# Kernel optimization log

Measured on AMD Instinct MI355X. Metric: run time of the kernel, lower is better.

## Reference

```python
import jax, jax.numpy as jnp
import numpy as np

N_NODES = 50000
GAMMA = -0.5
ZETA = 1.1
DEBUG_VAR = 1e-07


def setup_inputs() -> dict:
    key = jax.random.key(0)
    ks = jax.random.split(key, 8)
    N, E, D, H = N_NODES, 800000, 256, 128
    s = 0.05
    return {
        "x": jax.random.normal(ks[0], (N, D), jnp.float32),
        "W_nb": jax.random.normal(ks[1], (D, H), jnp.float32) * s,
        "b_nb": jnp.zeros((H,), jnp.float32),
        "W_self": jax.random.normal(ks[2], (D, H), jnp.float32) * s,
        "b_self": jnp.zeros((H,), jnp.float32),
        "W_att": jax.random.normal(ks[3], (2 * H, 1), jnp.float32) * s,
        "b_att": jnp.zeros((1,), jnp.float32),
        "values": jax.random.uniform(ks[4], (E,), jnp.float32),
        "noise": jax.random.uniform(ks[5], (E, 1), jnp.float32),
        "row": jax.random.randint(ks[6], (E,), 0, N, jnp.int32),
        "col": jax.random.randint(ks[7], (E,), 0, N, jnp.int32),
    }


def reference(x, W_nb, b_nb, W_self, b_self, W_att, b_att, values, noise, row, col):
    # edge gather + tiny attention MLP
    f1 = jax.nn.relu(x[row] @ W_nb + b_nb)      # [E, H]
    f2 = jax.nn.relu(x[col] @ W_self + b_self)  # [E, H]
    log_alpha = jnp.concatenate([f1, f2], axis=1) @ W_att + b_att  # [E, 1]

    # hard-concrete sample (training=True), beta=1.0
    u = noise + DEBUG_VAR
    gate = jax.nn.sigmoid(jnp.log(u) - jnp.log(1.0 - u) + log_alpha)
    mask = jnp.clip(gate * (ZETA - GAMMA) + GAMMA, 0.0, 1.0)[:, 0]  # [E]

    masked_values = values * mask

    # degree-normalized scatter: rowsum then symmetric D^{-1/2} A D^{-1/2}
    rowsum = jax.ops.segment_sum(masked_values, row, num_segments=N_NODES) + 1e-10
    d_inv_sqrt = jnp.power(rowsum, -0.5)
    d_inv_sqrt = jnp.where(jnp.isinf(d_inv_sqrt), 0.0, d_inv_sqrt)

    norm_values = masked_values * d_inv_sqrt[row] * d_inv_sqrt[col]  # [E]
    return norm_values
```

## Files before the change

kernel.cpp:

```cpp
#include <hip/hip_runtime.h>
#include <hip/hip_bf16.h>

typedef __attribute__((ext_vector_type(8))) short bf16x8;
typedef __attribute__((ext_vector_type(4))) float f32x4;

#define D_DIM 256
#define H_DIM 128
#define QSH 12544
#define NSL 64
#define NMAXL (4 * QSH)

__device__ inline ushort f2bf(float f) {
    union { float f; unsigned u; } a; a.f = f;
    unsigned r = a.u + 0x7fffu + ((a.u >> 16) & 1u);
    return (ushort)(r >> 16);
}
__device__ inline float bf2f(unsigned hi16) {
    union { unsigned u; float f; } a; a.u = hi16 << 16;
    return a.f;
}

__global__ void k0_init(const float* __restrict__ W_nb, const float* __restrict__ W_self,
                        ushort* __restrict__ Wt, float* __restrict__ dis, int N, int init_dis) {
    int i = blockIdx.x * 256 + threadIdx.x;
    if (i < 2 * H_DIM * D_DIM) {
        int j    = i & 7;
        int lane = (i >> 3) & 63;
        int ks   = (i >> 9) & 7;
        int ni   = (i >> 12) & 3;
        int cg   = i >> 14;
        int li   = lane & 15;
        int grp  = lane >> 4;
        int h    = (cg & 1) * 64 + ni * 16 + li;
        int k    = ks * 32 + grp * 8 + j;
        const float* W = (cg >> 1) ? W_self : W_nb;
        Wt[i] = f2bf(W[k * H_DIM + h]);
    }
    if (init_dis && i < N) dis[i] = 1e-10f;
}

__global__ __launch_bounds__(512, 2) void k1_gemm(
    const float* __restrict__ x, const ushort* __restrict__ Wt,
    const float* __restrict__ b_nb, const float* __restrict__ b_self,
    const float* __restrict__ W_att,
    float* __restrict__ g_nb, float* __restrict__ g_self, int N, int ntiles)
{
    __shared__ __align__(16) ushort A_lds[64][264];
    __shared__ float part[2][2][64];

    const int t    = threadIdx.x;
    const int lane = t & 63;
    const int w    = t >> 6;
    const int rh   = w >> 2;
    const int cg   = w & 3;
    const int br   = cg >> 1;
    const int ch   = cg & 1;
    const int li   = lane & 15;
    const int grp  = lane >> 4;

    float bias[4], aw[4];
    #pragma unroll
    for (int ni = 0; ni < 4; ni++) {
        int hh = ch * 64 + ni * 16 + li;
        bias[ni] = br ? b_self[hh] : b_nb[hh];
        aw[ni]   = W_att[br * H_DIM + hh];
    }

    bf16x8 Bf[4][8];
    #pragma unroll
    for (int ni = 0; ni < 4; ni++)
        #pragma unroll
        for (int ks = 0; ks < 8; ks++)
            Bf[ni][ks] = *reinterpret_cast<const bf16x8*>(
                Wt + (((size_t)(cg * 4 + ni) * 8 + ks) << 9) + lane * 8);

    const int sr = t >> 3;
    const int sc = t & 7;

    for (int rt = blockIdx.x; rt < ntiles; rt += gridDim.x) {
        const int row0 = rt * 64;

        __syncthreads();
        {
            const int gr = row0 + sr;
            const bool v = gr < N;
            const float4* src = reinterpret_cast<const float4*>(x + (size_t)gr * D_DIM);
            #pragma unroll
            for (int j = 0; j < 8; j++) {
                int c4 = sc + j * 8;
                ushort4 o;
                if (v) {
                    float4 f = src[c4];
                    o.x = f2bf(f.x); o.y = f2bf(f.y); o.z = f2bf(f.z); o.w = f2bf(f.w);
                } else { o.x = 0; o.y = 0; o.z = 0; o.w = 0; }
                *reinterpret_cast<ushort4*>(&A_lds[sr][c4 * 4]) = o;
            }
        }
        __syncthreads();

        f32x4 acc[2][4];
        #pragma unroll
        for (int mi = 0; mi < 2; mi++)
            #pragma unroll
            for (int ni = 0; ni < 4; ni++) acc[mi][ni] = f32x4{0.f, 0.f, 0.f, 0.f};

        #pragma unroll
        for (int ks = 0; ks < 8; ks++) {
            bf16x8 af0 = *reinterpret_cast<const bf16x8*>(&A_lds[rh * 32 + li][ks * 32 + grp * 8]);
            bf16x8 af1 = *reinterpret_cast<const bf16x8*>(&A_lds[rh * 32 + 16 + li][ks * 32 + grp * 8]);
            #pragma unroll
            for (int ni = 0; ni < 4; ni++) {
                acc[0][ni] = __builtin_amdgcn_mfma_f32_16x16x32_bf16(af0, Bf[ni][ks], acc[0][ni], 0, 0, 0);
                acc[1][ni] = __builtin_amdgcn_mfma_f32_16x16x32_bf16(af1, Bf[ni][ks], acc[1][ni], 0, 0, 0);
            }
        }

        float p[2][4];
        #pragma unroll
        for (int mi = 0; mi < 2; mi++)
            #pragma unroll
            for (int r4 = 0; r4 < 4; r4++) p[mi][r4] = 0.f;
        #pragma unroll
        for (int ni = 0; ni < 4; ni++)
            #pragma unroll
            for (int mi = 0; mi < 2; mi++)
                #pragma unroll
                for (int r4 = 0; r4 < 4; r4++) {
                    float y = acc[mi][ni][r4] + bias[ni];
                    y = y > 0.f ? y : 0.f;
                    p[mi][r4] += y * aw[ni];
                }
        #pragma unroll
        for (int mi = 0; mi < 2; mi++)
            #pragma unroll
            for (int r4 = 0; r4 < 4; r4++) {
                float v = p[mi][r4];
                #pragma unroll
                for (int m = 1; m < 16; m <<= 1) v += __shfl_xor(v, m);
                if (li == 0)
                    part[br][ch][rh * 32 + mi * 16 + grp * 4 + r4] = v;
            }
        __syncthreads();

        if (t < 128) {
            int b_ = t >> 6, lr = t & 63;
            int gr = row0 + lr;
            if (gr < N) {
                float val = part[b_][0][lr] + part[b_][1][lr];
                if (b_) g_self[gr] = val; else g_nb[gr] = val;
            }
        }
    }
}

__global__ __launch_bounds__(256) void k2a_gate(
    const int* __restrict__ row, const int* __restrict__ col,
    const float* __restrict__ values, const float* __restrict__ noise,
    const float* __restrict__ g_nb, const float* __restrict__ g_self,
    const float* __restrict__ b_att, unsigned* __restrict__ pk, int E)
{
    int i = (blockIdx.x * 256 + threadIdx.x) * 2;
    if (i >= E) return;
    const float ba = b_att[0];
    if (i + 1 < E) {
        int2   r2 = *reinterpret_cast<const int2*>(row + i);
        int2   c2 = *reinterpret_cast<const int2*>(col + i);
        float2 v2 = *reinterpret_cast<const float2*>(values + i);
        float2 u2 = *reinterpret_cast<const float2*>(noise + i);
        float gn0 = g_nb[r2.x], gs0 = g_self[c2.x];
        float gn1 = g_nb[r2.y], gs1 = g_self[c2.y];
        float u0 = u2.x + 1e-7f, u1 = u2.y + 1e-7f;
        float la0 = gn0 + gs0 + ba, la1 = gn1 + gs1 + ba;
        float g0 = u0 / (u0 + (1.f - u0) * __expf(-la0));
        float g1 = u1 / (u1 + (1.f - u1) * __expf(-la1));
        float m0 = v2.x * fminf(fmaxf(g0 * 1.6f - 0.5f, 0.f), 1.f);
        float m1 = v2.y * fminf(fmaxf(g1 * 1.6f - 0.5f, 0.f), 1.f);
        uint2 o;
        o.x = ((unsigned)r2.x << 16) | (unsigned)f2bf(m0);
        o.y = ((unsigned)r2.y << 16) | (unsigned)f2bf(m1);
        *reinterpret_cast<uint2*>(pk + i) = o;
    } else {
        int e = i;
        int   r = row[e];
        float u    = noise[e] + 1e-7f;
        float la   = g_nb[r] + g_self[col[e]] + ba;
        float gate = u / (u + (1.f - u) * __expf(-la));
        float mask = fminf(fmaxf(gate * 1.6f - 0.5f, 0.f), 1.f);
        pk[e] = ((unsigned)r << 16) | (unsigned)f2bf(values[e] * mask);
    }
}

__global__ __launch_bounds__(1024) void k2q_scatter(
    const unsigned* __restrict__ pk, ushort* __restrict__ priv, int E, int ES)
{
    __shared__ float acc[QSH];
    const int s  = blockIdx.x >> 2;
    const int q  = blockIdx.x & 3;
    const int t  = threadIdx.x;
    const int lo = q * QSH;

    for (int i = t; i < QSH; i += 1024) acc[i] = 0.f;
    __syncthreads();

    const int base = s * ES;
    int end = base + ES; if (end > E) end = E;

    int i = base + t * 4;
    for (; i + 3 < end; i += 4096) {
        uint4 p4 = *reinterpret_cast<const uint4*>(pk + i);
        unsigned p; int d; float m;
        p = p4.x; d = (int)(p >> 16) - lo; m = bf2f(p & 0xffffu);
        if ((unsigned)d < (unsigned)QSH && m != 0.f) atomicAdd(&acc[d], m);
        p = p4.y; d = (int)(p >> 16) - lo; m = bf2f(p & 0xffffu);
        if ((unsigned)d < (unsigned)QSH && m != 0.f) atomicAdd(&acc[d], m);
        p = p4.z; d = (int)(p >> 16) - lo; m = bf2f(p & 0xffffu);
        if ((unsigned)d < (unsigned)QSH && m != 0.f) atomicAdd(&acc[d], m);
        p = p4.w; d = (int)(p >> 16) - lo; m = bf2f(p & 0xffffu);
        if ((unsigned)d < (unsigned)QSH && m != 0.f) atomicAdd(&acc[d], m);
    }
    for (; i < end; i++) {
        unsigned p = pk[i];
        int d = (int)(p >> 16) - lo;
        float m = bf2f(p & 0xffffu);
        if ((unsigned)d < (unsigned)QSH && m != 0.f) atomicAdd(&acc[d], m);
    }
    __syncthreads();

    ushort* dst = priv + (size_t)s * (4 * QSH) + lo;
    for (int j = t * 2; j < QSH; j += 2048) {
        unsigned pkk = (unsigned)f2bf(acc[j]) | ((unsigned)f2bf(acc[j + 1]) << 16);
        *reinterpret_cast<unsigned*>(dst + j) = pkk;
    }
}

__global__ __launch_bounds__(256) void k2c_reduce(
    const ushort* __restrict__ priv, ushort* __restrict__ disb, int N)
{
    int n0 = (blockIdx.x * 256 + threadIdx.x) * 2;
    if (n0 >= N) return;
    float s0 = 1e-10f, s1 = 1e-10f;
    for (int p = 0; p < NSL; p++) {
        unsigned v = *reinterpret_cast<const unsigned*>(priv + (size_t)p * (4 * QSH) + n0);
        s0 += bf2f(v & 0xffffu);
        s1 += bf2f(v >> 16);
    }
    unsigned o = (unsigned)f2bf(rsqrtf(s0)) | ((unsigned)f2bf(rsqrtf(s1)) << 16);
    *reinterpret_cast<unsigned*>(disb + n0) = o;
}

__global__ __launch_bounds__(1024) void k3_edge2_lds(
    const unsigned* __restrict__ pk, const int* __restrict__ col,
    float* __restrict__ out, const ushort* __restrict__ disb,
    int Npad2, int E, int EB)
{
    __shared__ ushort ldis[NMAXL];
    const int t = threadIdx.x;
    {
        const unsigned* src = reinterpret_cast<const unsigned*>(disb);
        unsigned* dst = reinterpret_cast<unsigned*>(ldis);
        const int nw = Npad2 >> 1;
        for (int i = t; i < nw; i += 1024) dst[i] = src[i];
    }
    __syncthreads();

    const int base = blockIdx.x * EB;
    int end = base + EB; if (end > E) end = E;

    int i = base + t * 4;
    for (; i + 3 < end; i += 4096) {
        uint4 p4 = *reinterpret_cast<const uint4*>(pk + i);
        int4  c4 = *reinterpret_cast<const int4*>(col + i);
        float4 o;
        o.x = bf2f(p4.x & 0xffffu) * bf2f(ldis[p4.x >> 16]) * bf2f(ldis[c4.x]);
        o.y = bf2f(p4.y & 0xffffu) * bf2f(ldis[p4.y >> 16]) * bf2f(ldis[c4.y]);
        o.z = bf2f(p4.z & 0xffffu) * bf2f(ldis[p4.z >> 16]) * bf2f(ldis[c4.z]);
        o.w = bf2f(p4.w & 0xffffu) * bf2f(ldis[p4.w >> 16]) * bf2f(ldis[c4.w]);
        *reinterpret_cast<float4*>(out + i) = o;
    }
    for (; i < end; i++) {
        unsigned p = pk[i];
        out[i] = bf2f(p & 0xffffu) * bf2f(ldis[p >> 16]) * bf2f(ldis[col[i]]);
    }
}

__global__ __launch_bounds__(256) void k2_atomic_fb(
    const int* __restrict__ row, const int* __restrict__ col,
    const float* __restrict__ values, const float* __restrict__ noise,
    const float* __restrict__ g_nb, const float* __restrict__ g_self,
    const float* __restrict__ b_att,
    float* __restrict__ out, float* __restrict__ dis, int E)
{
    int e = blockIdx.x * 256 + threadIdx.x;
    if (e >= E) return;
    int   r = row[e], c = col[e];
    float u = noise[e] + 1e-7f;
    float la = g_nb[r] + g_self[c] + b_att[0];
    float gate = u / (u + (1.f - u) * __expf(-la));
    float mask = fminf(fmaxf(gate * 1.6f - 0.5f, 0.f), 1.f);
    float m = values[e] * mask;
    out[e] = m;
    if (m != 0.f) atomicAdd(&dis[r], m);
}
__global__ __launch_bounds__(256) void k2c_rsqrt_fb(float* __restrict__ dis, int N)
{
    int n = blockIdx.x * 256 + threadIdx.x;
    if (n < N) dis[n] = rsqrtf(dis[n]);
}
__global__ __launch_bounds__(256) void k3_edge2_fb(
    const int* __restrict__ row, const int* __restrict__ col,
    float* __restrict__ out, const float* __restrict__ dis, int E)
{
    int e = blockIdx.x * 256 + threadIdx.x;
    if (e >= E) return;
    out[e] = out[e] * dis[row[e]] * dis[col[e]];
}

extern "C" void kernel_launch(void* const* d_in, const int* in_sizes, int n_in,
                              void* d_out, int out_size, void* d_ws, size_t ws_size,
                              hipStream_t stream) {
    const float* x      = (const float*)d_in[0];
    const float* W_nb   = (const float*)d_in[1];
    const float* b_nb   = (const float*)d_in[2];
    const float* W_self = (const float*)d_in[3];
    const float* b_self = (const float*)d_in[4];
    const float* W_att  = (const float*)d_in[5];
    const float* b_att  = (const float*)d_in[6];
    const float* values = (const float*)d_in[7];
    const float* noise  = (const float*)d_in[8];
    const int*   row    = (const int*)d_in[9];
    const int*   col    = (const int*)d_in[10];

    const int N = in_sizes[0] / D_DIM;
    const int E = in_sizes[7];
    float* out = (float*)d_out;

    char* ws = (char*)d_ws;
    ushort* Wt     = (ushort*)ws;
    float*  g_nb   = (float*)(ws + 131072);
    float*  g_self = g_nb + N;
    float*  dis    = g_self + N;
    ushort* disb   = (ushort*)dis;
    ushort* priv   = (ushort*)(dis + N);
    size_t pk_off  = 131072 + (size_t)3 * N * 4 + (size_t)NSL * NMAXL * 2;
    pk_off = (pk_off + 15) & ~(size_t)15;
    unsigned* pk   = (unsigned*)(ws + pk_off);

    const int Npad2 = (N + 1) & ~1;
    int ES = ((E + NSL - 1) / NSL + 3) & ~3;
    size_t need = pk_off + (size_t)E * 4;
    bool lds_path = (N <= NMAXL) && (need <= ws_size);

    int init_n = 2 * H_DIM * D_DIM;
    if (N > init_n) init_n = N;
    k0_init<<<(init_n + 255) / 256, 256, 0, stream>>>(W_nb, W_self, Wt, dis, N, lds_path ? 0 : 1);

    const int ntiles = (N + 63) / 64;
    k1_gemm<<<ntiles, 512, 0, stream>>>(x, Wt, b_nb, b_self, W_att, g_nb, g_self, N, ntiles);

    if (lds_path) {
        int eb2 = ((E + 1) / 2 + 255) / 256;
        k2a_gate<<<eb2, 256, 0, stream>>>(row, col, values, noise, g_nb, g_self,
                                          b_att, pk, E);
        k2q_scatter<<<NSL * 4, 1024, 0, stream>>>(pk, priv, E, ES);
        k2c_reduce<<<((N + 1) / 2 + 255) / 256, 256, 0, stream>>>(priv, disb, N);
        int EB = ((E + 255) / 256 + 3) & ~3;
        k3_edge2_lds<<<256, 1024, 0, stream>>>(pk, col, out, disb, Npad2, E, EB);
    } else {
        k2_atomic_fb<<<(E + 255) / 256, 256, 0, stream>>>(row, col, values, noise,
                                                          g_nb, g_self, b_att, out, dis, E);
        k2c_rsqrt_fb<<<(N + 255) / 256, 256, 0, stream>>>(dis, N);
        k3_edge2_fb<<<(E + 255) / 256, 256, 0, stream>>>(row, col, out, dis, E);
    }
}
```

Measured before the change: 64.58 us.

## Make GEMM kernel persistent with register-prefetched next tile of x

The node GEMM kernel now launches a fixed grid of 256 blocks that loop over row tiles, rather than one block per tile. While computing the current tile, each thread loads the next tile's x rows into registers, then converts them to bf16 and writes them to LDS after the epilogue, so global loads overlap MFMA work. The per-block cost of loading the weight fragments is also amortized over several tiles. The trade-off is extra register pressure from the 8 float4 staging registers, and fewer blocks available to hide memory latency.

```diff
diff --git a/kernel.cpp b/kernel.cpp
--- a/kernel.cpp
+++ b/kernel.cpp
@@ -57,6 +57,7 @@
     const int ch   = cg & 1;
     const int li   = lane & 15;
     const int grp  = lane >> 4;
+    const int G    = gridDim.x;
 
     float bias[4], aw[4];
     #pragma unroll
@@ -77,26 +78,41 @@
     const int sr = t >> 3;
     const int sc = t & 7;
 
-    for (int rt = blockIdx.x; rt < ntiles; rt += gridDim.x) {
+    int rt = blockIdx.x;
+    if (rt >= ntiles) return;
+
+    {
+        const int gr = rt * 64 + sr;
+        const bool v = gr < N;
+        const float4* src = reinterpret_cast<const float4*>(x + (size_t)gr * D_DIM);
+        #pragma unroll
+        for (int j = 0; j < 8; j++) {
+            ushort4 o;
+            if (v) {
+                float4 f = src[sc + j * 8];
+                o.x = f2bf(f.x); o.y = f2bf(f.y); o.z = f2bf(f.z); o.w = f2bf(f.w);
+            } else { o.x = 0; o.y = 0; o.z = 0; o.w = 0; }
+            *reinterpret_cast<ushort4*>(&A_lds[sr][(sc + j * 8) * 4]) = o;
+        }
+    }
+    __syncthreads();
+
+    for (; rt < ntiles; rt += G) {
         const int row0 = rt * 64;
-
-        __syncthreads();
-        {
-            const int gr = row0 + sr;
-            const bool v = gr < N;
+        const int nxt  = rt + G;
+        const bool have_next = nxt < ntiles;
+
+        float4 stn[8];
+        bool nv = false;
+        if (have_next) {
+            const int gr = nxt * 64 + sr;
+            nv = gr < N;
             const float4* src = reinterpret_cast<const float4*>(x + (size_t)gr * D_DIM);
-            #pragma unroll
-            for (int j = 0; j < 8; j++) {
-                int c4 = sc + j * 8;
-                ushort4 o;
-                if (v) {
-                    float4 f = src[c4];
-                    o.x = f2bf(f.x); o.y = f2bf(f.y); o.z = f2bf(f.z); o.w = f2bf(f.w);
-                } else { o.x = 0; o.y = 0; o.z = 0; o.w = 0; }
-                *reinterpret_cast<ushort4*>(&A_lds[sr][c4 * 4]) = o;
+            if (nv) {
+                #pragma unroll
+                for (int j = 0; j < 8; j++) stn[j] = src[sc + j * 8];
             }
         }
-        __syncthreads();
 
         f32x4 acc[2][4];
         #pragma unroll
@@ -150,6 +166,18 @@
                 if (b_) g_self[gr] = val; else g_nb[gr] = val;
             }
         }
+        if (have_next) {
+            #pragma unroll
+            for (int j = 0; j < 8; j++) {
+                ushort4 o;
+                if (nv) {
+                    float4 f = stn[j];
+                    o.x = f2bf(f.x); o.y = f2bf(f.y); o.z = f2bf(f.z); o.w = f2bf(f.w);
+                } else { o.x = 0; o.y = 0; o.z = 0; o.w = 0; }
+                *reinterpret_cast<ushort4*>(&A_lds[sr][(sc + j * 8) * 4]) = o;
+            }
+        }
+        __syncthreads();
     }
 }
 
@@ -355,7 +383,7 @@
     k0_init<<<(init_n + 255) / 256, 256, 0, stream>>>(W_nb, W_self, Wt, dis, N, lds_path ? 0 : 1);
 
     const int ntiles = (N + 63) / 64;
-    k1_gemm<<<ntiles, 512, 0, stream>>>(x, Wt, b_nb, b_self, W_att, g_nb, g_self, N, ntiles);
+    k1_gemm<<<256, 512, 0, stream>>>(x, Wt, b_nb, b_self, W_att, g_nb, g_self, N, ntiles);
 
     if (lds_path) {
         int eb2 = ((E + 1) / 2 + 255) / 256;
```

New measurement: 56.38 us. 12.7% less time.
